# Kernel tuning notes

Measured on AMD Instinct MI355X. Metric: run time of the kernel, lower is better.

## Reference

```python
import jax, jax.numpy as jnp
import numpy as np

B, T, V = 16, 128, 64      # batch, input seq len, input vocab dim
E, H, DK = 512, 8, 64      # embed dim, heads, head dim (E // H)
WIN = 2
EPS = 1e-5                 # haiku LayerNorm eps


def setup_inputs() -> dict:
    key = jax.random.key(0)
    ks = jax.random.split(key, 32)
    n = lambda k, shape, s=0.02: (jax.random.normal(k, shape, jnp.float32) * s)
    return dict(
        x=jax.random.normal(ks[0], (B, T, V), jnp.float32),
        We=n(ks[1], (V, E)),
        eos_emb=n(ks[2], (E,)),
        Wq=n(ks[3], (E, H * DK), 0.05), bq=n(ks[4], (H * DK,)),
        Wk=n(ks[5], (E, H * DK), 0.05), bk=n(ks[6], (H * DK,)),
        Wv=n(ks[7], (E, H * DK), 0.05), bv=n(ks[8], (H * DK,)),
        Wo=n(ks[9], (H * DK, E), 0.05), bo=n(ks[10], (E,)),
        content_bias=n(ks[11], (H, DK)),
        relative_bias=n(ks[12], (H, DK)),
        pos_emb=n(ks[13], (2 * (WIN + 1) + 1, E)),
        ln2_s=jnp.ones((E,)), ln2_o=jnp.zeros((E,)),
        lno_s=jnp.ones((E,)), lno_o=jnp.zeros((E,)),
        W1=n(ks[14], (E, 2 * E), 0.05), b1=n(ks[15], (2 * E,)),
        W2=n(ks[16], (2 * E, E), 0.05), b2=n(ks[17], (E,)),
        Wh1=n(ks[18], (E, E), 0.05), bh1=n(ks[19], (E,)),
        Wh2=n(ks[20], (E, 2)),
    )


def _ln(y, s, o):
    m = jnp.mean(y, axis=-1, keepdims=True)
    v = jnp.var(y, axis=-1, keepdims=True)
    return (y - m) * s * jax.lax.rsqrt(v + EPS) + o


def reference(x, We, eos_emb, Wq, bq, Wk, bk, Wv, bv, Wo, bo,
              content_bias, relative_bias, pos_emb,
              ln2_s, ln2_o, lno_s, lno_o, W1, b1, W2, b2, Wh1, bh1, Wh2):
    b = x.shape[0]
    emb = x @ We                                              # [B,T,E]
    emb = jnp.concatenate(
        [emb, jnp.broadcast_to(eos_emb[None, None, :], (b, 1, E))], axis=1)
    S = emb.shape[1]                                          # T+1

    # relative-position keys are iteration-independent -> precompute once
    idxs = jnp.arange(S)
    rel_pos = jnp.clip(idxs[None, :] - idxs[:, None], -(WIN + 1), WIN + 1)
    rel_emb = pos_emb[rel_pos]                                # [S,S,E] (neg idx wraps, as original)
    rel_keys = (rel_emb @ Wk + bk).reshape(S, S, H, DK)       # [S,S,H,d]
    scale = np.float32(1.0 / np.sqrt(DK))

    def attn(h):
        q = (h @ Wq + bq).reshape(b, S, H, DK)
        k = (h @ Wk + bk).reshape(b, S, H, DK)
        v = (h @ Wv + bv).reshape(b, S, H, DK)
        cl = jnp.einsum('bthd,bThd->bhtT', q + content_bias, k)
        rl = jnp.einsum('bthd,Tthd->bhtT', q + relative_bias, rel_keys)
        w = jax.nn.softmax((cl + rl) * scale)
        a = jnp.einsum('bhtT,bThd->bthd', w, v).reshape(b, S, H * DK)
        return a @ Wo + bo

    halt_shift = jnp.array([2.0, -2.0], jnp.float32)

    def block(carry, _):
        h, lanh, lah, h_out = carry
        halted = jnp.exp(lah)[..., None]
        prev_h = h
        h = h + attn(h)
        hn = _ln(h, ln2_s, ln2_o)
        curr_h = h + (jax.nn.gelu(hn @ W1 + b1) @ W2 + b2)
        z = jnp.tanh(curr_h @ Wh1 + bh1) @ Wh2 + halt_shift
        log_g = jax.nn.log_softmax(z, axis=-1)
        # i < S-1 always holds for i in [0, T-2], so only the update branch runs
        log_halt = lanh + log_g[..., 1]
        lanh = lanh + log_g[..., 0]
        lah = jnp.logaddexp(lah, log_halt)
        curr_h = _ln(curr_h, lno_s, lno_o)
        h = halted * prev_h + (1.0 - halted) * curr_h
        h_out = h_out + jnp.exp(log_halt)[..., None] * curr_h
        return (h, lanh, lah, h_out), None

    h0 = _ln(emb, lno_s, lno_o)
    carry = (h0,
             jnp.zeros((b, S), jnp.float32),
             jnp.full((b, S), -64.0, jnp.float32),
             jnp.zeros_like(h0))
    (h, lanh, lah, h_out), _ = jax.lax.scan(block, carry, None, length=x.shape[1] - 1)
    return h_out
```

## Files before the change

### kernel.cpp

```cpp
#include <hip/hip_runtime.h>
#include <hip/hip_bf16.h>
#include <cstdint>
#include <cmath>

#define EPSLN 1e-5f

typedef __attribute__((ext_vector_type(8))) short bf16x8;
typedef __attribute__((ext_vector_type(4))) float f32x4;
typedef __attribute__((ext_vector_type(4))) unsigned short u16x4;

constexpr int Bc = 16;
constexpr int Sc = 129;
constexpr int Mc = Bc * Sc;
constexpr int MP = 2112;
constexpr int ITERS = 127;

__device__ __forceinline__ void gl2lds16(const void* g, void* l) {
    __builtin_amdgcn_global_load_lds(
        (const __attribute__((address_space(1))) unsigned int*)g,
        (__attribute__((address_space(3))) unsigned int*)l, 16, 0, 0);
}

template<int N> __device__ __forceinline__ void vmw() {
    if constexpr (N == 0) asm volatile("s_waitcnt vmcnt(0)" ::: "memory");
    else if constexpr (N == 3) asm volatile("s_waitcnt vmcnt(3)" ::: "memory");
    else if constexpr (N == 4) asm volatile("s_waitcnt vmcnt(4)" ::: "memory");
    else if constexpr (N == 6) asm volatile("s_waitcnt vmcnt(6)" ::: "memory");
}

__device__ __forceinline__ void bar() {
    __builtin_amdgcn_s_barrier();
    asm volatile("" ::: "memory");
}

__device__ __forceinline__ float bf2f(short s) {
    __hip_bfloat16 h;
    *reinterpret_cast<short*>(&h) = s;
    return __bfloat162float(h);
}
__device__ __forceinline__ short f2bf(float f) {
    __hip_bfloat16 h = __float2bfloat16(f);
    return *reinterpret_cast<short*>(&h);
}

template<int EPI, int BM>
__global__ __launch_bounds__(256)
void mgemm(const __hip_bfloat16* __restrict__ A, const __hip_bfloat16* __restrict__ Bt,
           const float* __restrict__ bias, const float* __restrict__ res,
           float* __restrict__ Cf, __hip_bfloat16* __restrict__ Cb,
           float* __restrict__ stats, const float* __restrict__ aux,
           int M, int N, int K)
{
    constexpr int ACH  = BM * 8;
    constexpr int ABYT = BM * 128;
    constexpr int STG  = ABYT + 8192;
    constexpr int LPT  = (ACH + 512) / 256;
    constexpr int NI   = (BM == 64) ? 2 : 1;
    __shared__ char lds[2 * STG];
    const int tid = threadIdx.x;
    const int bm = blockIdx.y * BM, bn = blockIdx.x << 6;
    const int lane = tid & 63, wv = tid >> 6;
    const int wm = (BM == 64) ? ((wv & 1) << 5) : 0;
    const int wn = (BM == 64) ? ((wv >> 1) << 5) : (wv << 4);
    const int fr = lane & 15, kg = lane >> 4;

    int offA[2][2], offB[2][2];
    #pragma unroll
    for (int mi = 0; mi < 2; ++mi)
        #pragma unroll
        for (int kk = 0; kk < 2; ++kk) {
            int kb = (kk << 6) + (kg << 4);
            int ra = wm + (mi << 4) + fr;
            offA[mi][kk] = (ra << 7) + (kb ^ ((ra & 7) << 4));
        }
    #pragma unroll
    for (int ni = 0; ni < NI; ++ni)
        #pragma unroll
        for (int kk = 0; kk < 2; ++kk) {
            int kb = (kk << 6) + (kg << 4);
            int rb = wn + (ni << 4) + fr;
            offB[ni][kk] = ABYT + (rb << 7) + (kb ^ ((rb & 7) << 4));
        }

    auto stage = [&](int sb, int k0) {
        char* base = lds + sb * STG;
        #pragma unroll
        for (int c = 0; c < ACH / 256; ++c) {
            int idx = c * 256 + tid;
            int row = idx >> 3, kb = (idx & 7) << 4;
            gl2lds16((const char*)A + (((size_t)(bm + row) * K + k0) << 1) + (kb ^ ((row & 7) << 4)),
                     base + idx * 16);
        }
        #pragma unroll
        for (int c = 0; c < 2; ++c) {
            int idx = c * 256 + tid;
            int row = idx >> 3, kb = (idx & 7) << 4;
            gl2lds16((const char*)Bt + (((size_t)(bn + row) * K + k0) << 1) + (kb ^ ((row & 7) << 4)),
                     base + ABYT + idx * 16);
        }
    };

    f32x4 acc[2][2] = {};
    const int NK = K >> 6;
    stage(0, 0);
    for (int ks = 0; ks < NK; ++ks) {
        const int cur = ks & 1;
        if (ks + 1 < NK) { stage(cur ^ 1, (ks + 1) << 6); vmw<LPT>(); }
        else vmw<0>();
        bar();
        const char* bp = lds + cur * STG;
        bf16x8 af[2][2], bf_[2][2];
        #pragma unroll
        for (int mi = 0; mi < 2; ++mi)
            #pragma unroll
            for (int kk = 0; kk < 2; ++kk)
                af[mi][kk] = *(const bf16x8*)(bp + offA[mi][kk]);
        #pragma unroll
        for (int ni = 0; ni < NI; ++ni)
            #pragma unroll
            for (int kk = 0; kk < 2; ++kk)
                bf_[ni][kk] = *(const bf16x8*)(bp + offB[ni][kk]);
        #pragma unroll
        for (int kk = 0; kk < 2; ++kk)
            #pragma unroll
            for (int mi = 0; mi < 2; ++mi)
                #pragma unroll
                for (int ni = 0; ni < NI; ++ni)
                    acc[mi][ni] = __builtin_amdgcn_mfma_f32_16x16x32_bf16(
                        af[mi][kk], bf_[ni][kk], acc[mi][ni], 0, 0, 0);
        asm volatile("s_waitcnt lgkmcnt(0)" ::: "memory");
        bar();
    }

    const int rb4 = kg << 2;
    float b_[NI], w_[NI];
    #pragma unroll
    for (int ni = 0; ni < NI; ++ni) {
        int col = bn + wn + (ni << 4) + fr;
        b_[ni] = bias[col];
        if (EPI == 6) w_[ni] = aux[col];
    }
    #pragma unroll
    for (int mi = 0; mi < 2; ++mi)
        #pragma unroll
        for (int r = 0; r < 4; ++r) {
            const int row = bm + wm + (mi << 4) + rb4 + r;
            if (row >= M) continue;
            float mean = 0.f, rinv = 0.f;
            if (EPI == 6) {
                float s0 = stats[row * 2 + 0], s1 = stats[row * 2 + 1];
                mean = s0 * (1.f / 512.f);
                rinv = rsqrtf(s1 * (1.f / 512.f) - mean * mean + EPSLN);
            }
            float vs = 0.f, vq = 0.f;
            #pragma unroll
            for (int ni = 0; ni < NI; ++ni) {
                const int col = bn + wn + (ni << 4) + fr;
                float v = acc[mi][ni][r];
                if (EPI == 6) v = rinv * v - mean * rinv * w_[ni] + b_[ni];
                else v += b_[ni];
                if (EPI == 4 || EPI == 5) v += res[(size_t)row * N + col];
                if (EPI == 6) {
                    float g = 0.5f * v * (1.f + tanhf(0.7978845608028654f * (v + 0.044715f * v * v * v)));
                    Cb[(size_t)row * N + col] = __float2bfloat16(g);
                } else if (EPI == 3) {
                    Cb[(size_t)row * N + col] = __float2bfloat16(v);
                } else if (EPI == 4) {
                    Cf[(size_t)row * N + col] = v;
                    Cb[(size_t)row * N + col] = __float2bfloat16(v);
                } else if (EPI == 5) {
                    Cf[(size_t)row * N + col] = v;
                    Cb[(size_t)row * N + col] = __float2bfloat16(v);
                    vs += v; vq += v * v;
                } else {
                    Cf[(size_t)row * N + col] = v;
                }
            }
            if (EPI == 5) {
                #pragma unroll
                for (int m2 = 1; m2 < 16; m2 <<= 1) {
                    vs += __shfl_xor(vs, m2);
                    vq += __shfl_xor(vq, m2);
                }
                if (fr == 0) {
                    atomicAdd(&stats[row * 2 + 0], vs);
                    atomicAdd(&stats[row * 2 + 1], vq);
                }
            }
        }
}

__global__ __launch_bounds__(256)
void halt_gemm(const __hip_bfloat16* __restrict__ Ahp, const __hip_bfloat16* __restrict__ Bhp,
               const float* __restrict__ bh1, const float* __restrict__ Wh2,
               float* __restrict__ z, int M)
{
    constexpr int STG = 12288;
    __shared__ char lds[2 * STG];
    const int tid = threadIdx.x;
    const int bm = blockIdx.y << 5, bn = blockIdx.x << 6;
    const int lane = tid & 63, wv = tid >> 6;
    const int wn = wv << 4;
    const int fr = lane & 15, kg = lane >> 4;

    int offA[2][2], offB[2];
    #pragma unroll
    for (int mi = 0; mi < 2; ++mi)
        #pragma unroll
        for (int kk = 0; kk < 2; ++kk) {
            int kb = (kk << 6) + (kg << 4);
            int ra = (mi << 4) + fr;
            offA[mi][kk] = (ra << 7) + (kb ^ ((ra & 7) << 4));
        }
    #pragma unroll
    for (int kk = 0; kk < 2; ++kk) {
        int kb = (kk << 6) + (kg << 4);
        int rb = wn + fr;
        offB[kk] = 4096 + (rb << 7) + (kb ^ ((rb & 7) << 4));
    }

    auto stage = [&](int sb, int k0) {
        char* base = lds + sb * STG;
        {
            int row = tid >> 3, kb = (tid & 7) << 4;
            int swz = kb ^ ((row & 7) << 4);
            size_t aoff = (((size_t)(bm + row) * 512 + k0) << 1) + swz;
            gl2lds16((const char*)Ahp + aoff, base + tid * 16);
        }
        #pragma unroll
        for (int c = 0; c < 2; ++c) {
            int idx = c * 256 + tid;
            int row = idx >> 3, kb = (idx & 7) << 4;
            int swz = kb ^ ((row & 7) << 4);
            size_t boff = (((size_t)(bn + row) * 512 + k0) << 1) + swz;
            gl2lds16((const char*)Bhp + boff, base + 4096 + idx * 16);
        }
    };

    f32x4 acc[2] = {};
    stage(0, 0);
    for (int ks = 0; ks < 8; ++ks) {
        const int cur = ks & 1;
        if (ks < 7) { stage(cur ^ 1, (ks + 1) << 6); vmw<3>(); }
        else vmw<0>();
        bar();
        const char* bp = lds + cur * STG;
        bf16x8 ah[2][2], bh_[2];
        #pragma unroll
        for (int mi = 0; mi < 2; ++mi)
            #pragma unroll
            for (int kk = 0; kk < 2; ++kk)
                ah[mi][kk] = *(const bf16x8*)(bp + offA[mi][kk]);
        #pragma unroll
        for (int kk = 0; kk < 2; ++kk)
            bh_[kk] = *(const bf16x8*)(bp + offB[kk]);
        #pragma unroll
        for (int kk = 0; kk < 2; ++kk)
            #pragma unroll
            for (int mi = 0; mi < 2; ++mi)
                acc[mi] = __builtin_amdgcn_mfma_f32_16x16x32_bf16(ah[mi][kk], bh_[kk], acc[mi], 0, 0, 0);
        asm volatile("s_waitcnt lgkmcnt(0)" ::: "memory");
        bar();
    }

    const int col = bn + wn + fr;
    const float b_ = bh1[col];
    const float w0_ = Wh2[col * 2 + 0];
    const float w1_ = Wh2[col * 2 + 1];
    #pragma unroll
    for (int mi = 0; mi < 2; ++mi)
        #pragma unroll
        for (int r = 0; r < 4; ++r) {
            float v = tanhf(acc[mi][r] + b_);
            float p0 = v * w0_;
            float p1 = v * w1_;
            #pragma unroll
            for (int m2 = 1; m2 < 16; m2 <<= 1) {
                p0 += __shfl_xor(p0, m2);
                p1 += __shfl_xor(p1, m2);
            }
            if (fr == 0) {
                int row = bm + (mi << 4) + (kg << 2) + r;
                if (row < M) {
                    atomicAdd(&z[row * 2 + 0], p0);
                    atomicAdd(&z[row * 2 + 1], p1);
                }
            }
        }
}

#define KT_BASE 0
#define P_BASE  0
#define VT_BASE 18432
#define QC_BASE 43008
#define R_BASE  47616
#define WM_BASE 48640
#define WS_BASE 49152
__global__ __launch_bounds__(256)
void attn_mfma(const __hip_bfloat16* __restrict__ qkvb,
               const float* __restrict__ rk7, const float* __restrict__ cbias,
               const float* __restrict__ rbias, __hip_bfloat16* __restrict__ aout)
{
    __shared__ char lds[49664];
    const int tid = threadIdx.x;
    const int chunk = blockIdx.x, hh = blockIdx.y, b = blockIdx.z;
    const int q0 = chunk << 5;
    const int lane = tid & 63, wv = tid >> 6;
    const int fr = lane & 15, kg = lane >> 4;
    const size_t qrow0 = (size_t)b * Sc;
    const short* qs = (const short*)qkvb;

    {
        f32x4 zz = {};
        #pragma unroll
        for (int i = 0; i < 6; ++i)
            *(f32x4*)(lds + VT_BASE + (i * 256 + tid) * 16) = zz;
        if (tid < 120)
            *(f32x4*)(lds + KT_BASE + 129 * 128 + tid * 16) = zz;
    }
    __syncthreads();

    #pragma unroll
    for (int i = 0; i < 5; ++i) {
        int idx = i * 256 + tid;
        if (idx < 1152) {
            int row = idx >> 3, ch = idx & 7;
            if (row <= 128) {
                const char* src = (const char*)qkvb +
                    (((qrow0 + row) * 1536 + 512 + (size_t)hh * 64) << 1) + ((ch ^ (row & 7)) << 4);
                gl2lds16(src, lds + KT_BASE + idx * 16);
            }
        }
    }
    #pragma unroll
    for (int i = 0; i < 5; ++i) {
        int idx = i * 256 + tid;
        if (idx < 1032) {
            int T = idx >> 3, g = idx & 7;
            bf16x8 v = *(const bf16x8*)(qs + (qrow0 + T) * 1536 + 1024 + hh * 64 + g * 8);
            #pragma unroll
            for (int j = 0; j < 8; ++j) {
                int row = g * 8 + j;
                int key = (g ^ j) & 7;
                *(short*)(lds + VT_BASE + row * 384 + ((T * 2) ^ (key << 4))) = v[j];
            }
        }
    }
    {
        int row = tid >> 3, g = tid & 7;
        bf16x8 q8 = *(const bf16x8*)(qs + (qrow0 + q0 + row) * 1536 + hh * 64 + g * 8);
        const float* cb = cbias + hh * 64 + g * 8;
        bf16x8 o8;
        #pragma unroll
        for (int j = 0; j < 8; ++j)
            o8[j] = f2bf(bf2f(q8[j]) + cb[j]);
        *(bf16x8*)(lds + QC_BASE + row * 144 + g * 16) = o8;
    }
    if (tid < 224) {
        int row = tid / 7, c = tid % 7;
        const short* qp = qs + (qrow0 + q0 + row) * 1536 + hh * 64;
        const float* rp  = rk7 + c * 512 + hh * 64;
        const float* rbp = rbias + hh * 64;
        float a = 0.f;
        #pragma unroll
        for (int g = 0; g < 8; ++g) {
            bf16x8 q8 = *(const bf16x8*)(qp + g * 8);
            #pragma unroll
            for (int j = 0; j < 8; ++j)
                a += (bf2f(q8[j]) + rbp[g * 8 + j]) * rp[g * 8 + j];
        }
        *(float*)(lds + R_BASE + (row * 8 + c) * 4) = a;
    }
    __syncthreads();

    f32x4 acc[2][3] = {};
    __builtin_amdgcn_s_setprio(1);
    #pragma unroll
    for (int ni = 0; ni < 3; ++ni) {
        int nt = wv + ni * 4;
        if (nt > 8) continue;
        #pragma unroll
        for (int mt = 0; mt < 2; ++mt)
            #pragma unroll
            for (int ks = 0; ks < 2; ++ks) {
                bf16x8 a = *(const bf16x8*)(lds + QC_BASE + (mt * 16 + fr) * 144 + ks * 64 + kg * 16);
                int rowb = nt * 16 + fr;
                bf16x8 bb = *(const bf16x8*)(lds + KT_BASE + rowb * 128 +
                                             ((ks * 64 + kg * 16) ^ ((rowb & 7) << 4)));
                acc[mt][ni] = __builtin_amdgcn_mfma_f32_16x16x32_bf16(a, bb, acc[mt][ni], 0, 0, 0);
            }
    }
    __builtin_amdgcn_s_setprio(0);

    #pragma unroll
    for (int ni = 0; ni < 3; ++ni) {
        int nt = wv + ni * 4;
        int col = nt * 16 + fr;
        #pragma unroll
        for (int mt = 0; mt < 2; ++mt)
            #pragma unroll
            for (int r = 0; r < 4; ++r) {
                int row = mt * 16 + kg * 4 + r;
                float sv = -1e30f;
                if (nt <= 8 && col <= 128) {
                    int delta = q0 + row - col;
                    int c = delta >= 3 ? 3 : (delta <= -3 ? 4 : (delta < 0 ? delta + 7 : delta));
                    float rl = *(const float*)(lds + R_BASE + (row * 8 + c) * 4);
                    sv = (acc[mt][ni][r] + rl) * 0.125f;
                }
                acc[mt][ni][r] = sv;
            }
    }

    float m_[2][4];
    #pragma unroll
    for (int mt = 0; mt < 2; ++mt)
        #pragma unroll
        for (int r = 0; r < 4; ++r) {
            float m = fmaxf(fmaxf(acc[mt][0][r], acc[mt][1][r]), acc[mt][2][r]);
            #pragma unroll
            for (int b2 = 1; b2 < 16; b2 <<= 1) m = fmaxf(m, __shfl_xor(m, b2));
            m_[mt][r] = m;
        }
    if (fr == 0) {
        float* wm = (float*)(lds + WM_BASE) + (wv << 5);
        #pragma unroll
        for (int mt = 0; mt < 2; ++mt)
            #pragma unroll
            for (int r = 0; r < 4; ++r)
                wm[mt * 16 + (kg << 2) + r] = m_[mt][r];
    }
    __syncthreads();

    if (tid < 128) {
        int row = tid >> 2;
        *(double*)(lds + P_BASE + row * 336 + 288 + (tid & 3) * 8) = 0.0;
    }

    const float* wm = (const float*)(lds + WM_BASE);
    float gm[2][4], su[2][4];
    #pragma unroll
    for (int mt = 0; mt < 2; ++mt)
        #pragma unroll
        for (int r = 0; r < 4; ++r) {
            int row = mt * 16 + (kg << 2) + r;
            float g0 = fmaxf(wm[row], wm[32 + row]);
            float g1 = fmaxf(wm[64 + row], wm[96 + row]);
            gm[mt][r] = fmaxf(g0, g1);
            su[mt][r] = 0.f;
        }
    #pragma unroll
    for (int ni = 0; ni < 3; ++ni)
        #pragma unroll
        for (int mt = 0; mt < 2; ++mt)
            #pragma unroll
            for (int r = 0; r < 4; ++r) {
                float s = acc[mt][ni][r];
                float e = (s > -1e29f) ? expf(s - gm[mt][r]) : 0.f;
                acc[mt][ni][r] = e;
                su[mt][r] += e;
            }
    #pragma unroll
    for (int mt = 0; mt < 2; ++mt)
        #pragma unroll
        for (int r = 0; r < 4; ++r) {
            float s = su[mt][r];
            #pragma unroll
            for (int b2 = 1; b2 < 16; b2 <<= 1) s += __shfl_xor(s, b2);
            su[mt][r] = s;
        }
    if (fr == 0) {
        float* ws = (float*)(lds + WS_BASE) + (wv << 5);
        #pragma unroll
        for (int mt = 0; mt < 2; ++mt)
            #pragma unroll
            for (int r = 0; r < 4; ++r)
                ws[mt * 16 + (kg << 2) + r] = su[mt][r];
    }
    __syncthreads();

    const float* wsm = (const float*)(lds + WS_BASE);
    float inv_[2][4];
    #pragma unroll
    for (int mt = 0; mt < 2; ++mt)
        #pragma unroll
        for (int r = 0; r < 4; ++r) {
            int row = mt * 16 + (kg << 2) + r;
            float t = (wsm[row] + wsm[32 + row]) + (wsm[64 + row] + wsm[96 + row]);
            inv_[mt][r] = 1.f / t;
        }
    #pragma unroll
    for (int ni = 0; ni < 3; ++ni) {
        int nt = wv + ni * 4;
        if (nt > 8) continue;
        int col = nt * 16 + fr;
        #pragma unroll
        for (int mt = 0; mt < 2; ++mt)
            #pragma unroll
            for (int r = 0; r < 4; ++r) {
                int row = mt * 16 + (kg << 2) + r;
                *(short*)(lds + P_BASE + row * 336 + col * 2) =
                    f2bf(acc[mt][ni][r] * inv_[mt][r]);
            }
    }
    __syncthreads();

    f32x4 acc2[2] = {};
    const int rowv = wv * 16 + fr;
    const int keyv = ((rowv >> 3) ^ rowv) & 7;
    __builtin_amdgcn_s_setprio(1);
    #pragma unroll
    for (int mt = 0; mt < 2; ++mt)
        #pragma unroll
        for (int ks = 0; ks < 5; ++ks) {
            bf16x8 a  = *(const bf16x8*)(lds + P_BASE + (mt * 16 + fr) * 336 + ks * 64 + kg * 16);
            bf16x8 bb = *(const bf16x8*)(lds + VT_BASE + rowv * 384 +
                                         ((ks * 64 + kg * 16) ^ (keyv << 4)));
            acc2[mt] = __builtin_amdgcn_mfma_f32_16x16x32_bf16(a, bb, acc2[mt], 0, 0, 0);
        }
    __builtin_amdgcn_s_setprio(0);
    #pragma unroll
    for (int mt = 0; mt < 2; ++mt)
        #pragma unroll
        for (int r = 0; r < 4; ++r) {
            int t = q0 + mt * 16 + kg * 4 + r;
            if (t <= 128)
                aout[(qrow0 + t) * 512 + hh * 64 + wv * 16 + fr] = __float2bfloat16(acc2[mt][r]);
        }
}

__global__ __launch_bounds__(256)
void haltblend(const float* __restrict__ curr, const float* __restrict__ s,
               const float* __restrict__ o, float* __restrict__ zbuf,
               float* __restrict__ lanh, float* __restrict__ lah,
               float* __restrict__ h, __hip_bfloat16* __restrict__ hb,
               float* __restrict__ hout, float* __restrict__ stats)
{
    const int row = (blockIdx.x << 2) + (threadIdx.x >> 6);
    const int lane = threadIdx.x & 63;

    float z0 = zbuf[row * 2 + 0] + 2.f;
    float z1 = zbuf[row * 2 + 1] - 2.f;
    float mxz = fmaxf(z0, z1);
    float lse = mxz + logf(expf(z0 - mxz) + expf(z1 - mxz));
    float lg0 = z0 - lse, lg1 = z1 - lse;
    float ln_ = lanh[row], la_ = lah[row];
    float lhalt = ln_ + lg1;
    float hl = expf(la_);
    float ph = expf(lhalt);

    const size_t rbase = (size_t)row * 512;
    const int c0 = lane << 3;
    f32x4 x0 = *(const f32x4*)(curr + rbase + c0);
    f32x4 x1 = *(const f32x4*)(curr + rbase + c0 + 4);
    float sum = (x0[0] + x0[1]) + (x0[2] + x0[3]) + (x1[0] + x1[1]) + (x1[2] + x1[3]);
    float sq  = (x0[0] * x0[0] + x0[1] * x0[1]) + (x0[2] * x0[2] + x0[3] * x0[3])
              + (x1[0] * x1[0] + x1[1] * x1[1]) + (x1[2] * x1[2] + x1[3] * x1[3]);
    #pragma unroll
    for (int m2 = 1; m2 < 64; m2 <<= 1) { sum += __shfl_xor(sum, m2); sq += __shfl_xor(sq, m2); }
    float mean = sum * (1.f / 512.f);
    float inv = rsqrtf(sq * (1.f / 512.f) - mean * mean + EPSLN);

    if (lane == 0) {
        lanh[row] = ln_ + lg0;
        float m3 = fmaxf(la_, lhalt);
        lah[row] = m3 + logf(expf(la_ - m3) + expf(lhalt - m3));
        zbuf[row * 2 + 0] = 0.f;
        zbuf[row * 2 + 1] = 0.f;
        stats[row * 2 + 0] = 0.f;
        stats[row * 2 + 1] = 0.f;
    }

    f32x4 sv0 = *(const f32x4*)(s + c0), sv1 = *(const f32x4*)(s + c0 + 4);
    f32x4 ov0 = *(const f32x4*)(o + c0), ov1 = *(const f32x4*)(o + c0 + 4);
    f32x4 hv0 = *(f32x4*)(h + rbase + c0), hv1 = *(f32x4*)(h + rbase + c0 + 4);
    f32x4 ho0 = *(f32x4*)(hout + rbase + c0), ho1 = *(f32x4*)(hout + rbase + c0 + 4);
    u16x4 hb0, hb1;
    #pragma unroll
    for (int e = 0; e < 4; ++e) {
        float cl = (x0[e] - mean) * inv * sv0[e] + ov0[e];
        float hn = hl * hv0[e] + (1.f - hl) * cl;
        hv0[e] = hn;
        __hip_bfloat16 bb = __float2bfloat16(hn);
        hb0[e] = *reinterpret_cast<unsigned short*>(&bb);
        ho0[e] += ph * cl;
    }
    #pragma unroll
    for (int e = 0; e < 4; ++e) {
        float cl = (x1[e] - mean) * inv * sv1[e] + ov1[e];
        float hn = hl * hv1[e] + (1.f - hl) * cl;
        hv1[e] = hn;
        __hip_bfloat16 bb = __float2bfloat16(hn);
        hb1[e] = *reinterpret_cast<unsigned short*>(&bb);
        ho1[e] += ph * cl;
    }
    *(f32x4*)(h + rbase + c0) = hv0;
    *(f32x4*)(h + rbase + c0 + 4) = hv1;
    *(u16x4*)(reinterpret_cast<unsigned short*>(hb) + rbase + c0) = hb0;
    *(u16x4*)(reinterpret_cast<unsigned short*>(hb) + rbase + c0 + 4) = hb1;
    *(f32x4*)(hout + rbase + c0) = ho0;
    *(f32x4*)(hout + rbase + c0 + 4) = ho1;
}

__global__ __launch_bounds__(256)
void emb_kernel(const float* __restrict__ x, const float* __restrict__ We,
                const float* __restrict__ eos, const float* __restrict__ s,
                const float* __restrict__ o, float* __restrict__ h,
                __hip_bfloat16* __restrict__ hb)
{
    int row = blockIdx.x, tid = threadIdx.x;
    int b = row / Sc, t = row % Sc;
    __shared__ float xs[64];
    if (t != 128 && tid < 64) xs[tid] = x[((size_t)b * 128 + t) * 64 + tid];
    __syncthreads();
    float v0, v1;
    if (t == 128) {
        v0 = eos[tid]; v1 = eos[tid + 256];
    } else {
        v0 = 0.f; v1 = 0.f;
        #pragma unroll 8
        for (int k = 0; k < 64; ++k) {
            float xv = xs[k];
            v0 = fmaf(xv, We[k * 512 + tid], v0);
            v1 = fmaf(xv, We[k * 512 + tid + 256], v1);
        }
    }
    float sum = v0 + v1, sq = v0 * v0 + v1 * v1;
    #pragma unroll
    for (int m2 = 1; m2 < 64; m2 <<= 1) { sum += __shfl_xor(sum, m2); sq += __shfl_xor(sq, m2); }
    __shared__ float ssum[4], ssq[4];
    if ((tid & 63) == 0) { ssum[tid >> 6] = sum; ssq[tid >> 6] = sq; }
    __syncthreads();
    float tot = ssum[0] + ssum[1] + ssum[2] + ssum[3];
    float totq = ssq[0] + ssq[1] + ssq[2] + ssq[3];
    float mean = tot * (1.f / 512.f);
    float inv = rsqrtf(totq * (1.f / 512.f) - mean * mean + EPSLN);
    float h0 = (v0 - mean) * inv * s[tid] + o[tid];
    float h1 = (v1 - mean) * inv * s[tid + 256] + o[tid + 256];
    h[(size_t)row * 512 + tid] = h0;
    h[(size_t)row * 512 + tid + 256] = h1;
    hb[(size_t)row * 512 + tid] = __float2bfloat16(h0);
    hb[(size_t)row * 512 + tid + 256] = __float2bfloat16(h1);
}

__global__ __launch_bounds__(256)
void rk7_kernel(const float* __restrict__ pos, const float* __restrict__ Wk,
                const float* __restrict__ bk, float* __restrict__ rk7)
{
    int c = blockIdx.x, tid = threadIdx.x;
    __shared__ float ps[512];
    ps[tid] = pos[c * 512 + tid];
    ps[tid + 256] = pos[c * 512 + tid + 256];
    __syncthreads();
    float a0 = bk[tid], a1 = bk[tid + 256];
    for (int k = 0; k < 512; ++k) {
        float pv = ps[k];
        a0 = fmaf(pv, Wk[(size_t)k * 512 + tid], a0);
        a1 = fmaf(pv, Wk[(size_t)k * 512 + tid + 256], a1);
    }
    rk7[c * 512 + tid] = a0;
    rk7[c * 512 + tid + 256] = a1;
}

__global__ __launch_bounds__(256)
void pack_qkvT(const float* __restrict__ Wq, const float* __restrict__ Wk,
               const float* __restrict__ Wv, __hip_bfloat16* __restrict__ Wt)
{
    int idx = blockIdx.x * 256 + threadIdx.x;
    if (idx >= 1536 * 512) return;
    int n = idx >> 9, k = idx & 511;
    const float* src = (n < 512) ? Wq : (n < 1024) ? Wk : Wv;
    int nc = n & 511;
    Wt[idx] = __float2bfloat16(src[(size_t)k * 512 + nc]);
}

__global__ __launch_bounds__(256)
void transposeT(const float* __restrict__ W, __hip_bfloat16* __restrict__ Wt, int K, int N)
{
    int idx = blockIdx.x * 256 + threadIdx.x;
    if (idx >= K * N) return;
    int n = idx / K, k = idx - n * K;
    Wt[idx] = __float2bfloat16(W[(size_t)k * N + n]);
}

__global__ __launch_bounds__(256)
void transposeT_scale(const float* __restrict__ W, const float* __restrict__ s,
                      __hip_bfloat16* __restrict__ Wt, int K, int N)
{
    int idx = blockIdx.x * 256 + threadIdx.x;
    if (idx >= K * N) return;
    int n = idx / K, k = idx - n * K;
    Wt[idx] = __float2bfloat16(W[(size_t)k * N + n] * s[k]);
}

__global__ __launch_bounds__(256)
void fold_w1(const float* __restrict__ W, const float* __restrict__ s,
             const float* __restrict__ o, const float* __restrict__ b,
             float* __restrict__ w1sum, float* __restrict__ b1f, int K, int N)
{
    int n = blockIdx.x * 256 + threadIdx.x;
    if (n >= N) return;
    float ws = 0.f, bo_ = b[n];
    for (int k = 0; k < K; ++k) {
        float w = W[(size_t)k * N + n];
        ws = fmaf(s[k], w, ws);
        bo_ = fmaf(o[k], w, bo_);
    }
    w1sum[n] = ws;
    b1f[n] = bo_;
}

__global__ __launch_bounds__(256)
void pack_bias(const float* __restrict__ bq, const float* __restrict__ bk,
               const float* __restrict__ bv, float* __restrict__ bqkv)
{
    int idx = blockIdx.x * 256 + threadIdx.x;
    if (idx < 1536)
        bqkv[idx] = (idx < 512) ? bq[idx] : (idx < 1024) ? bk[idx - 512] : bv[idx - 1024];
}

__global__ __launch_bounds__(256)
void init_kernel(float* __restrict__ lanh, float* __restrict__ lah,
                 float* __restrict__ zbuf, float* __restrict__ stats)
{
    int idx = blockIdx.x * 256 + threadIdx.x;
    if (idx < Mc) {
        lanh[idx] = 0.f; lah[idx] = -64.f;
        zbuf[idx * 2 + 0] = 0.f; zbuf[idx * 2 + 1] = 0.f;
    }
    if (idx < MP) {
        stats[idx * 2 + 0] = 0.f; stats[idx * 2 + 1] = 0.f;
    }
}

extern "C" void kernel_launch(void* const* d_in, const int* in_sizes, int n_in,
                              void* d_out, int out_size, void* d_ws, size_t ws_size,
                              hipStream_t stream)
{
    const float* x     = (const float*)d_in[0];
    const float* We    = (const float*)d_in[1];
    const float* eos   = (const float*)d_in[2];
    const float* Wq    = (const float*)d_in[3];
    const float* bq    = (const float*)d_in[4];
    const float* Wk    = (const float*)d_in[5];
    const float* bk    = (const float*)d_in[6];
    const float* Wv    = (const float*)d_in[7];
    const float* bv    = (const float*)d_in[8];
    const float* Wo    = (const float*)d_in[9];
    const float* bo    = (const float*)d_in[10];
    const float* cbias = (const float*)d_in[11];
    const float* rbias = (const float*)d_in[12];
    const float* pos   = (const float*)d_in[13];
    const float* ln2s  = (const float*)d_in[14];
    const float* ln2o  = (const float*)d_in[15];
    const float* lnos  = (const float*)d_in[16];
    const float* lnoo  = (const float*)d_in[17];
    const float* W1    = (const float*)d_in[18];
    const float* b1    = (const float*)d_in[19];
    const float* W2    = (const float*)d_in[20];
    const float* b2    = (const float*)d_in[21];
    const float* Wh1   = (const float*)d_in[22];
    const float* bh1   = (const float*)d_in[23];
    const float* Wh2   = (const float*)d_in[24];
    (void)in_sizes; (void)n_in; (void)ws_size;

    char* wp = (char*)d_ws;
    auto alloc = [&](size_t bytes) { char* p = wp; wp += (bytes + 255) & ~(size_t)255; return p; };
    float*          h     = (float*)alloc((size_t)MP * 512 * 4);
    __hip_bfloat16* hb    = (__hip_bfloat16*)alloc((size_t)MP * 512 * 2);
    __hip_bfloat16* qkvb  = (__hip_bfloat16*)alloc((size_t)MP * 1536 * 2);
    __hip_bfloat16* abufb = (__hip_bfloat16*)alloc((size_t)MP * 512 * 2);
    float*          hmid  = (float*)alloc((size_t)MP * 512 * 4);
    __hip_bfloat16* hmidb = (__hip_bfloat16*)alloc((size_t)MP * 512 * 2);
    __hip_bfloat16* g1b   = (__hip_bfloat16*)alloc((size_t)MP * 1024 * 2);
    float*          curr  = (float*)alloc((size_t)MP * 512 * 4);
    __hip_bfloat16* chi   = (__hip_bfloat16*)alloc((size_t)MP * 512 * 2);
    __hip_bfloat16* WqkvT = (__hip_bfloat16*)alloc((size_t)1536 * 512 * 2);
    __hip_bfloat16* WoT   = (__hip_bfloat16*)alloc((size_t)512 * 512 * 2);
    __hip_bfloat16* W1T   = (__hip_bfloat16*)alloc((size_t)1024 * 512 * 2);
    __hip_bfloat16* W2T   = (__hip_bfloat16*)alloc((size_t)512 * 1024 * 2);
    __hip_bfloat16* Wh1Th = (__hip_bfloat16*)alloc((size_t)512 * 512 * 2);
    float*          bqkv  = (float*)alloc(1536 * 4);
    float*          w1sum = (float*)alloc(1024 * 4);
    float*          b1f   = (float*)alloc(1024 * 4);
    float*          rk7   = (float*)alloc(7 * 512 * 4);
    float*          lanh  = (float*)alloc(Mc * 4);
    float*          lah   = (float*)alloc(Mc * 4);
    float*          zbuf  = (float*)alloc((size_t)Mc * 2 * 4);
    float*          stats = (float*)alloc((size_t)MP * 2 * 4);
    float* hout = (float*)d_out;

    hipMemsetAsync(d_out, 0, (size_t)out_size * sizeof(float), stream);
    init_kernel<<<(MP + 255) / 256, 256, 0, stream>>>(lanh, lah, zbuf, stats);
    pack_qkvT<<<(1536 * 512 + 255) / 256, 256, 0, stream>>>(Wq, Wk, Wv, WqkvT);
    transposeT<<<(512 * 512 + 255) / 256, 256, 0, stream>>>(Wo, WoT, 512, 512);
    transposeT_scale<<<(512 * 1024 + 255) / 256, 256, 0, stream>>>(W1, ln2s, W1T, 512, 1024);
    fold_w1<<<4, 256, 0, stream>>>(W1, ln2s, ln2o, b1, w1sum, b1f, 512, 1024);
    transposeT<<<(1024 * 512 + 255) / 256, 256, 0, stream>>>(W2, W2T, 1024, 512);
    transposeT<<<(512 * 512 + 255) / 256, 256, 0, stream>>>(Wh1, Wh1Th, 512, 512);
    pack_bias<<<(1536 + 255) / 256, 256, 0, stream>>>(bq, bk, bv, bqkv);
    rk7_kernel<<<7, 256, 0, stream>>>(pos, Wk, bk, rk7);
    emb_kernel<<<Mc, 256, 0, stream>>>(x, We, eos, lnos, lnoo, h, hb);

    for (int it = 0; it < ITERS; ++it) {
        mgemm<3, 64><<<dim3(24, 33), 256, 0, stream>>>(
            hb, WqkvT, bqkv, nullptr, nullptr, qkvb, nullptr, nullptr, Mc, 1536, 512);
        attn_mfma<<<dim3(5, 8, 16), 256, 0, stream>>>(qkvb, rk7, cbias, rbias, abufb);
        mgemm<5, 32><<<dim3(8, 66), 256, 0, stream>>>(
            abufb, WoT, bo, h, hmid, hmidb, stats, nullptr, Mc, 512, 512);
        mgemm<6, 64><<<dim3(16, 33), 256, 0, stream>>>(
            hmidb, W1T, b1f, nullptr, nullptr, g1b, stats, w1sum, Mc, 1024, 512);
        mgemm<4, 32><<<dim3(8, 66), 256, 0, stream>>>(
            g1b, W2T, b2, hmid, curr, chi, nullptr, nullptr, Mc, 512, 1024);
        halt_gemm<<<dim3(8, 66), 256, 0, stream>>>(chi, Wh1Th, bh1, Wh2, zbuf, Mc);
        haltblend<<<Mc / 4, 256, 0, stream>>>(curr, lnos, lnoo, zbuf, lanh, lah, h, hb, hout, stats);
    }
}
```

Before: 10.72 ms.

## Use 128-row tiles for QKV GEMM and merge attention softmax reductions

The mgemm kernel gains a BM=128 variant in which each wave owns a 64x32 output tile (4x2 MFMA fragments), with A-row loads clamped at M. The QKV projection switches to it, halving the grid along M and reusing each B tile across more rows. Separately, the attention softmax now computes each wave's local max, exponentials and partial sums in one pass and combines them across waves with a rescaling step, which removes one __syncthreads and a round trip through LDS. The larger tile raises register and LDS use per block and leaves fewer blocks to fill the GPU.

```diff
diff --git a/kernel.cpp b/kernel.cpp
--- a/kernel.cpp
+++ b/kernel.cpp
@@ -55,18 +55,19 @@
     constexpr int ABYT = BM * 128;
     constexpr int STG  = ABYT + 8192;
     constexpr int LPT  = (ACH + 512) / 256;
-    constexpr int NI   = (BM == 64) ? 2 : 1;
+    constexpr int NI   = (BM >= 64) ? 2 : 1;
+    constexpr int MI   = (BM == 128) ? 4 : 2;
     __shared__ char lds[2 * STG];
     const int tid = threadIdx.x;
     const int bm = blockIdx.y * BM, bn = blockIdx.x << 6;
     const int lane = tid & 63, wv = tid >> 6;
-    const int wm = (BM == 64) ? ((wv & 1) << 5) : 0;
-    const int wn = (BM == 64) ? ((wv >> 1) << 5) : (wv << 4);
+    const int wm = (BM == 128) ? ((wv & 1) << 6) : (BM == 64) ? ((wv & 1) << 5) : 0;
+    const int wn = (BM >= 64) ? ((wv >> 1) << 5) : (wv << 4);
     const int fr = lane & 15, kg = lane >> 4;
 
-    int offA[2][2], offB[2][2];
-    #pragma unroll
-    for (int mi = 0; mi < 2; ++mi)
+    int offA[MI][2], offB[NI][2];
+    #pragma unroll
+    for (int mi = 0; mi < MI; ++mi)
         #pragma unroll
         for (int kk = 0; kk < 2; ++kk) {
             int kb = (kk << 6) + (kg << 4);
@@ -88,7 +89,9 @@
         for (int c = 0; c < ACH / 256; ++c) {
             int idx = c * 256 + tid;
             int row = idx >> 3, kb = (idx & 7) << 4;
-            gl2lds16((const char*)A + (((size_t)(bm + row) * K + k0) << 1) + (kb ^ ((row & 7) << 4)),
+            int gr = bm + row;
+            if (BM == 128) gr = gr < M ? gr : (M - 1);
+            gl2lds16((const char*)A + (((size_t)gr * K + k0) << 1) + (kb ^ ((row & 7) << 4)),
                      base + idx * 16);
         }
         #pragma unroll
@@ -100,7 +103,7 @@
         }
     };
 
-    f32x4 acc[2][2] = {};
+    f32x4 acc[MI][NI] = {};
     const int NK = K >> 6;
     stage(0, 0);
     for (int ks = 0; ks < NK; ++ks) {
@@ -109,9 +112,9 @@
         else vmw<0>();
         bar();
         const char* bp = lds + cur * STG;
-        bf16x8 af[2][2], bf_[2][2];
-        #pragma unroll
-        for (int mi = 0; mi < 2; ++mi)
+        bf16x8 af[MI][2], bf_[NI][2];
+        #pragma unroll
+        for (int mi = 0; mi < MI; ++mi)
             #pragma unroll
             for (int kk = 0; kk < 2; ++kk)
                 af[mi][kk] = *(const bf16x8*)(bp + offA[mi][kk]);
@@ -123,7 +126,7 @@
         #pragma unroll
         for (int kk = 0; kk < 2; ++kk)
             #pragma unroll
-            for (int mi = 0; mi < 2; ++mi)
+            for (int mi = 0; mi < MI; ++mi)
                 #pragma unroll
                 for (int ni = 0; ni < NI; ++ni)
                     acc[mi][ni] = __builtin_amdgcn_mfma_f32_16x16x32_bf16(
@@ -141,7 +144,7 @@
         if (EPI == 6) w_[ni] = aux[col];
     }
     #pragma unroll
-    for (int mi = 0; mi < 2; ++mi)
+    for (int mi = 0; mi < MI; ++mi)
         #pragma unroll
         for (int r = 0; r < 4; ++r) {
             const int row = bm + wm + (mi << 4) + rb4 + r;
@@ -412,7 +415,7 @@
             }
     }
 
-    float m_[2][4];
+    float m_[2][4], su[2][4];
     #pragma unroll
     for (int mt = 0; mt < 2; ++mt)
         #pragma unroll
@@ -421,14 +424,38 @@
             #pragma unroll
             for (int b2 = 1; b2 < 16; b2 <<= 1) m = fmaxf(m, __shfl_xor(m, b2));
             m_[mt][r] = m;
+            su[mt][r] = 0.f;
+        }
+    #pragma unroll
+    for (int ni = 0; ni < 3; ++ni)
+        #pragma unroll
+        for (int mt = 0; mt < 2; ++mt)
+            #pragma unroll
+            for (int r = 0; r < 4; ++r) {
+                float s = acc[mt][ni][r];
+                float e = (s > -1e29f) ? expf(s - m_[mt][r]) : 0.f;
+                acc[mt][ni][r] = e;
+                su[mt][r] += e;
+            }
+    #pragma unroll
+    for (int mt = 0; mt < 2; ++mt)
+        #pragma unroll
+        for (int r = 0; r < 4; ++r) {
+            float s = su[mt][r];
+            #pragma unroll
+            for (int b2 = 1; b2 < 16; b2 <<= 1) s += __shfl_xor(s, b2);
+            su[mt][r] = s;
         }
     if (fr == 0) {
         float* wm = (float*)(lds + WM_BASE) + (wv << 5);
+        float* ws = (float*)(lds + WS_BASE) + (wv << 5);
         #pragma unroll
         for (int mt = 0; mt < 2; ++mt)
             #pragma unroll
-            for (int r = 0; r < 4; ++r)
+            for (int r = 0; r < 4; ++r) {
                 wm[mt * 16 + (kg << 2) + r] = m_[mt][r];
+                ws[mt * 16 + (kg << 2) + r] = su[mt][r];
+            }
     }
     __syncthreads();
 
@@ -437,57 +464,20 @@
         *(double*)(lds + P_BASE + row * 336 + 288 + (tid & 3) * 8) = 0.0;
     }
 
-    const float* wm = (const float*)(lds + WM_BASE);
-    float gm[2][4], su[2][4];
+    const float* wmv = (const float*)(lds + WM_BASE);
+    const float* wsv = (const float*)(lds + WS_BASE);
+    float fac[2][4];
     #pragma unroll
     for (int mt = 0; mt < 2; ++mt)
         #pragma unroll
         for (int r = 0; r < 4; ++r) {
             int row = mt * 16 + (kg << 2) + r;
-            float g0 = fmaxf(wm[row], wm[32 + row]);
-            float g1 = fmaxf(wm[64 + row], wm[96 + row]);
-            gm[mt][r] = fmaxf(g0, g1);
-            su[mt][r] = 0.f;
-        }
-    #pragma unroll
-    for (int ni = 0; ni < 3; ++ni)
-        #pragma unroll
-        for (int mt = 0; mt < 2; ++mt)
-            #pragma unroll
-            for (int r = 0; r < 4; ++r) {
-                float s = acc[mt][ni][r];
-                float e = (s > -1e29f) ? expf(s - gm[mt][r]) : 0.f;
-                acc[mt][ni][r] = e;
-                su[mt][r] += e;
-            }
-    #pragma unroll
-    for (int mt = 0; mt < 2; ++mt)
-        #pragma unroll
-        for (int r = 0; r < 4; ++r) {
-            float s = su[mt][r];
-            #pragma unroll
-            for (int b2 = 1; b2 < 16; b2 <<= 1) s += __shfl_xor(s, b2);
-            su[mt][r] = s;
-        }
-    if (fr == 0) {
-        float* ws = (float*)(lds + WS_BASE) + (wv << 5);
-        #pragma unroll
-        for (int mt = 0; mt < 2; ++mt)
-            #pragma unroll
-            for (int r = 0; r < 4; ++r)
-                ws[mt * 16 + (kg << 2) + r] = su[mt][r];
-    }
-    __syncthreads();
-
-    const float* wsm = (const float*)(lds + WS_BASE);
-    float inv_[2][4];
-    #pragma unroll
-    for (int mt = 0; mt < 2; ++mt)
-        #pragma unroll
-        for (int r = 0; r < 4; ++r) {
-            int row = mt * 16 + (kg << 2) + r;
-            float t = (wsm[row] + wsm[32 + row]) + (wsm[64 + row] + wsm[96 + row]);
-            inv_[mt][r] = 1.f / t;
+            float m0 = wmv[row],      m1 = wmv[32 + row];
+            float m2 = wmv[64 + row], m3 = wmv[96 + row];
+            float gm = fmaxf(fmaxf(m0, m1), fmaxf(m2, m3));
+            float tot = wsv[row] * expf(m0 - gm) + wsv[32 + row] * expf(m1 - gm)
+                      + wsv[64 + row] * expf(m2 - gm) + wsv[96 + row] * expf(m3 - gm);
+            fac[mt][r] = expf(m_[mt][r] - gm) / tot;
         }
     #pragma unroll
     for (int ni = 0; ni < 3; ++ni) {
@@ -500,7 +490,7 @@
             for (int r = 0; r < 4; ++r) {
                 int row = mt * 16 + (kg << 2) + r;
                 *(short*)(lds + P_BASE + row * 336 + col * 2) =
-                    f2bf(acc[mt][ni][r] * inv_[mt][r]);
+                    f2bf(acc[mt][ni][r] * fac[mt][r]);
             }
     }
     __syncthreads();
@@ -803,7 +793,7 @@
     emb_kernel<<<Mc, 256, 0, stream>>>(x, We, eos, lnos, lnoo, h, hb);
 
     for (int it = 0; it < ITERS; ++it) {
-        mgemm<3, 64><<<dim3(24, 33), 256, 0, stream>>>(
+        mgemm<3, 128><<<dim3(24, 17), 256, 0, stream>>>(
             hb, WqkvT, bqkv, nullptr, nullptr, qkvb, nullptr, nullptr, Mc, 1536, 512);
         attn_mfma<<<dim3(5, 8, 16), 256, 0, stream>>>(qkvb, rk7, cbias, rbias, abufb);
         mgemm<5, 32><<<dim3(8, 66), 256, 0, stream>>>(
```

After: 11.12 ms. 1.04x slower.

## Fold relative-position logits into QKV GEMM as extra output columns

Applied to the files above, without the earlier changes.

Precomputes Wq·rk7 per head and relative slot (plus the bias terms) into 64 extra columns of the packed QKV weight, so the QKV GEMM directly emits per-row relative logits in fp32. The attention kernel then just loads these 7 values per row instead of recomputing a 64-wide dot product from bf16 q for each query, slot and head block. This adds one more column tile to the GEMM grid and changes rounding slightly, since the logits now come from the bf16 h GEMM rather than from bf16 q plus the fp32 bias.

```diff
diff --git a/kernel.cpp b/kernel.cpp
--- a/kernel.cpp
+++ b/kernel.cpp
@@ -164,7 +164,8 @@
                     float g = 0.5f * v * (1.f + tanhf(0.7978845608028654f * (v + 0.044715f * v * v * v)));
                     Cb[(size_t)row * N + col] = __float2bfloat16(g);
                 } else if (EPI == 3) {
-                    Cb[(size_t)row * N + col] = __float2bfloat16(v);
+                    if (col < 1536) Cb[(size_t)row * 1536 + col] = __float2bfloat16(v);
+                    else            Cf[(size_t)row * 64 + (col - 1536)] = v;
                 } else if (EPI == 4) {
                     Cf[(size_t)row * N + col] = v;
                     Cb[(size_t)row * N + col] = __float2bfloat16(v);
@@ -298,8 +299,8 @@
 #define WS_BASE 49152
 __global__ __launch_bounds__(256)
 void attn_mfma(const __hip_bfloat16* __restrict__ qkvb,
-               const float* __restrict__ rk7, const float* __restrict__ cbias,
-               const float* __restrict__ rbias, __hip_bfloat16* __restrict__ aout)
+               const float* __restrict__ rl, const float* __restrict__ cbias,
+               __hip_bfloat16* __restrict__ aout)
 {
     __shared__ char lds[49664];
     const int tid = threadIdx.x;
@@ -358,18 +359,8 @@
     }
     if (tid < 224) {
         int row = tid / 7, c = tid % 7;
-        const short* qp = qs + (qrow0 + q0 + row) * 1536 + hh * 64;
-        const float* rp  = rk7 + c * 512 + hh * 64;
-        const float* rbp = rbias + hh * 64;
-        float a = 0.f;
-        #pragma unroll
-        for (int g = 0; g < 8; ++g) {
-            bf16x8 q8 = *(const bf16x8*)(qp + g * 8);
-            #pragma unroll
-            for (int j = 0; j < 8; ++j)
-                a += (bf2f(q8[j]) + rbp[g * 8 + j]) * rp[g * 8 + j];
-        }
-        *(float*)(lds + R_BASE + (row * 8 + c) * 4) = a;
+        *(float*)(lds + R_BASE + (row * 8 + c) * 4) =
+            rl[(qrow0 + q0 + row) * 64 + hh * 8 + c];
     }
     __syncthreads();
 
@@ -405,8 +396,8 @@
                 if (nt <= 8 && col <= 128) {
                     int delta = q0 + row - col;
                     int c = delta >= 3 ? 3 : (delta <= -3 ? 4 : (delta < 0 ? delta + 7 : delta));
-                    float rl = *(const float*)(lds + R_BASE + (row * 8 + c) * 4);
-                    sv = (acc[mt][ni][r] + rl) * 0.125f;
+                    float rlv = *(const float*)(lds + R_BASE + (row * 8 + c) * 4);
+                    sv = (acc[mt][ni][r] + rlv) * 0.125f;
                 }
                 acc[mt][ni][r] = sv;
             }
@@ -672,6 +663,33 @@
     const float* src = (n < 512) ? Wq : (n < 1024) ? Wk : Wv;
     int nc = n & 511;
     Wt[idx] = __float2bfloat16(src[(size_t)k * 512 + nc]);
+}
+
+__global__ __launch_bounds__(256)
+void fold_rl(const float* __restrict__ Wq, const float* __restrict__ bq,
+             const float* __restrict__ rbias, const float* __restrict__ rk7,
+             __hip_bfloat16* __restrict__ Wt, float* __restrict__ bqkv)
+{
+    int idx = blockIdx.x * 256 + threadIdx.x;
+    if (idx >= 64 * 512) return;
+    int n = idx >> 9, k = idx & 511;
+    int hh = n >> 3, c = n & 7;
+    float a = 0.f;
+    if (c < 7) {
+        #pragma unroll 8
+        for (int d = 0; d < 64; ++d)
+            a = fmaf(Wq[(size_t)k * 512 + hh * 64 + d], rk7[c * 512 + hh * 64 + d], a);
+    }
+    Wt[(size_t)(1536 + n) * 512 + k] = __float2bfloat16(a);
+    if (idx < 64) {
+        int hh2 = idx >> 3, c2 = idx & 7;
+        float s = 0.f;
+        if (c2 < 7) {
+            for (int d = 0; d < 64; ++d)
+                s = fmaf(bq[hh2 * 64 + d] + rbias[hh2 * 64 + d], rk7[c2 * 512 + hh2 * 64 + d], s);
+        }
+        bqkv[1536 + idx] = s;
+    }
 }
 
 __global__ __launch_bounds__(256)
@@ -769,18 +787,19 @@
     float*          h     = (float*)alloc((size_t)MP * 512 * 4);
     __hip_bfloat16* hb    = (__hip_bfloat16*)alloc((size_t)MP * 512 * 2);
     __hip_bfloat16* qkvb  = (__hip_bfloat16*)alloc((size_t)MP * 1536 * 2);
+    float*          rlb   = (float*)alloc((size_t)MP * 64 * 4);
     __hip_bfloat16* abufb = (__hip_bfloat16*)alloc((size_t)MP * 512 * 2);
     float*          hmid  = (float*)alloc((size_t)MP * 512 * 4);
     __hip_bfloat16* hmidb = (__hip_bfloat16*)alloc((size_t)MP * 512 * 2);
     __hip_bfloat16* g1b   = (__hip_bfloat16*)alloc((size_t)MP * 1024 * 2);
     float*          curr  = (float*)alloc((size_t)MP * 512 * 4);
     __hip_bfloat16* chi   = (__hip_bfloat16*)alloc((size_t)MP * 512 * 2);
-    __hip_bfloat16* WqkvT = (__hip_bfloat16*)alloc((size_t)1536 * 512 * 2);
+    __hip_bfloat16* WqkvT = (__hip_bfloat16*)alloc((size_t)1600 * 512 * 2);
     __hip_bfloat16* WoT   = (__hip_bfloat16*)alloc((size_t)512 * 512 * 2);
     __hip_bfloat16* W1T   = (__hip_bfloat16*)alloc((size_t)1024 * 512 * 2);
     __hip_bfloat16* W2T   = (__hip_bfloat16*)alloc((size_t)512 * 1024 * 2);
     __hip_bfloat16* Wh1Th = (__hip_bfloat16*)alloc((size_t)512 * 512 * 2);
-    float*          bqkv  = (float*)alloc(1536 * 4);
+    float*          bqkv  = (float*)alloc(1600 * 4);
     float*          w1sum = (float*)alloc(1024 * 4);
     float*          b1f   = (float*)alloc(1024 * 4);
     float*          rk7   = (float*)alloc(7 * 512 * 4);
@@ -800,12 +819,13 @@
     transposeT<<<(512 * 512 + 255) / 256, 256, 0, stream>>>(Wh1, Wh1Th, 512, 512);
     pack_bias<<<(1536 + 255) / 256, 256, 0, stream>>>(bq, bk, bv, bqkv);
     rk7_kernel<<<7, 256, 0, stream>>>(pos, Wk, bk, rk7);
+    fold_rl<<<(64 * 512 + 255) / 256, 256, 0, stream>>>(Wq, bq, rbias, rk7, WqkvT, bqkv);
     emb_kernel<<<Mc, 256, 0, stream>>>(x, We, eos, lnos, lnoo, h, hb);
 
     for (int it = 0; it < ITERS; ++it) {
-        mgemm<3, 64><<<dim3(24, 33), 256, 0, stream>>>(
-            hb, WqkvT, bqkv, nullptr, nullptr, qkvb, nullptr, nullptr, Mc, 1536, 512);
-        attn_mfma<<<dim3(5, 8, 16), 256, 0, stream>>>(qkvb, rk7, cbias, rbias, abufb);
+        mgemm<3, 64><<<dim3(25, 33), 256, 0, stream>>>(
+            hb, WqkvT, bqkv, nullptr, rlb, qkvb, nullptr, nullptr, Mc, 1600, 512);
+        attn_mfma<<<dim3(5, 8, 16), 256, 0, stream>>>(qkvb, rlb, cbias, abufb);
         mgemm<5, 32><<<dim3(8, 66), 256, 0, stream>>>(
             abufb, WoT, bo, h, hmid, hmidb, stats, nullptr, Mc, 512, 512);
         mgemm<6, 64><<<dim3(16, 33), 256, 0, stream>>>(
```

Result: faster. 9.652 ms (-9.9%).
